# Kernel tuning notes

Measured on AMD Instinct MI355X. Metric: run time of the kernel, lower is better.

The kernel has to match this reference:

```python
import jax, jax.numpy as jnp
import numpy as np

ROW_PENALTY = 1.0
BIG = 9999.0
K = 8  # torch.topk(scores, 8, largest=False)


def _completion_loss(X, H, C, Mf, M):
    # X,H,C: [T,D] float; Mf: float mask; M: int mask (constant)
    T, D = H.shape
    diff = H[:, None, :] - H[None, :, :]                 # [T,T,D]
    # masked_select condition: (M[i]*M[j]) >= 0 per feature
    P = (Mf[:, None, :] * Mf[None, :, :]) >= 0           # [T,T,D] bool
    Pf = P.astype(H.dtype)
    n = Pf.sum(-1)                                       # [T,T] masked count
    s1 = (Pf * diff).sum(-1)                             # masked sum
    s2 = (Pf * diff * diff).sum(-1)                      # masked sum of squares
    mean = s1 / n
    # torch.var default is unbiased (n-1 denominator)
    var = (s2 - n * mean * mean) / (n - 1.0)
    # score only computed when i != j and (M[i] != M[j]).any(); else stays 9999
    valid = (M[:, None, :] != M[None, :, :]).any(-1) & (~jnp.eye(T, dtype=bool))
    scores = jnp.where(valid, jnp.sqrt(jnp.where(valid, var, 1.0)), BIG)
    # smallest-K via top_k on negated scores
    neg_vals, idx = jax.lax.top_k(-scores, K)            # [T,K]
    topk = -neg_vals
    w = jax.nn.softmax(-topk, axis=-1)                   # Softmax(dim=0) over the K-vector
    d2 = H[:, None, :] - H[idx]                          # [T,K,D]
    norms = jnp.sqrt((d2 * d2).sum(-1))                  # torch.norm(H[i]-H[j])
    row_loss = (w * norms).sum()
    mse = jnp.sum((X * Mf - (H - C) * Mf) ** 2)          # MSELoss(reduction='sum')
    return mse + ROW_PENALTY * row_loss


def setup_inputs() -> dict:
    key = jax.random.key(0)
    k1, k2, k3, k4 = jax.random.split(key, 4)
    T, D = 512, 256
    X = jax.random.normal(k1, (T, D), jnp.float32)
    H = jax.random.normal(k2, (T, D), jnp.float32)
    C = jax.random.normal(k3, (T, D), jnp.float32)
    M = jax.random.randint(k4, (T, D), 0, 2, jnp.int32)  # binary observation mask
    return {"X": X, "H": H, "C": C, "M": M, "T": T}


def reference(X, H, C, M, T):
    Mf = M.astype(X.dtype)
    return _completion_loss(X, H, C, Mf, M)
```

## Files before the change

kernel.cpp:

```cpp
#include <hip/hip_runtime.h>
#include <math.h>

#define TT 512
#define DD 256
#define BIGF 9999.0f
#define KK 8

typedef unsigned long long ull;
typedef __attribute__((ext_vector_type(8))) short s16x8;
typedef __attribute__((ext_vector_type(4))) float f32x4;

#define HB_OFF   0
#define G_OFF    262144
#define A_OFF    1310720
#define B_OFF    1312768
#define MB_OFF   1314816
#define MSEP_OFF 1331200

__device__ __forceinline__ unsigned short toBf16(float f) {
  unsigned int u = __float_as_uint(f);
  unsigned int r = u + 0x7FFFu + ((u >> 16) & 1u);
  return (unsigned short)(r >> 16);
}

__global__ __launch_bounds__(256) void prep_kernel(
    const float* __restrict__ X, const float* __restrict__ H,
    const float* __restrict__ C, const int* __restrict__ M,
    unsigned short* __restrict__ Hb, float* __restrict__ A,
    float* __restrict__ B, ull* __restrict__ MB, float* __restrict__ MSEP4,
    float* __restrict__ out) {
  const int b = blockIdx.x;
  const int t = threadIdx.x;
  const int wid = t >> 6, lane = t & 63;
  const int i0 = 4 * b;
  if (b == 0 && t == 0) out[0] = 0.0f;

  __shared__ float sA[4][4], sB[4][4], sM[4][4];
#pragma unroll
  for (int r = 0; r < 4; ++r) {
    const int row = i0 + r;
    const int idx = row * DD + t;
    const float x = X[idx], h = H[idx], c = C[idx];
    const int m = M[idx];
    const int dstk = t ^ ((row & 7) << 3);
    Hb[row * DD + dstk] = toBf16(h);
    const float e = m ? (x - h + c) : 0.0f;
    float pm = e * e, ph = h, ph2 = h * h;
#pragma unroll
    for (int s = 1; s < 64; s <<= 1) {
      pm  += __shfl_xor(pm, s);
      ph  += __shfl_xor(ph, s);
      ph2 += __shfl_xor(ph2, s);
    }
    const ull bal = __ballot(m != 0);
    if (lane == 0) {
      sA[r][wid] = ph; sB[r][wid] = ph2; sM[r][wid] = pm;
      MB[row * 4 + wid] = bal;
    }
  }
  __syncthreads();
  if (t < 4) {
    A[i0 + t] = sA[t][0] + sA[t][1] + sA[t][2] + sA[t][3];
    B[i0 + t] = sB[t][0] + sB[t][1] + sB[t][2] + sB[t][3];
  }
  if (t == 0) {
    float ms = 0.0f;
#pragma unroll
    for (int r = 0; r < 4; ++r)
#pragma unroll
      for (int wq = 0; wq < 4; ++wq) ms += sM[r][wq];
    MSEP4[b] = ms;
  }
}

__global__ __launch_bounds__(256, 2) void gram_kernel(
    const unsigned short* __restrict__ Hb, float* __restrict__ G) {
  __shared__ unsigned short At[64 * 256];
  __shared__ unsigned short Bt[64 * 256];
  const int t = threadIdx.x;
  const int lane = t & 63;
  const int wv = t >> 6;
  const int bx = blockIdx.x & 7, by = blockIdx.x >> 3;
  const int i0 = 64 * by, j0 = 64 * bx;

  {
    const s16x8* __restrict__ sa = (const s16x8*)(Hb + i0 * DD);
    const s16x8* __restrict__ sb = (const s16x8*)(Hb + j0 * DD);
    s16x8 va[8], vb[8];
#pragma unroll
    for (int q = 0; q < 8; ++q) va[q] = sa[q * 256 + t];
#pragma unroll
    for (int q = 0; q < 8; ++q) vb[q] = sb[q * 256 + t];
    s16x8* da = (s16x8*)At;
    s16x8* db = (s16x8*)Bt;
#pragma unroll
    for (int q = 0; q < 8; ++q) da[q * 256 + t] = va[q];
#pragma unroll
    for (int q = 0; q < 8; ++q) db[q * 256 + t] = vb[q];
  }
  __syncthreads();

  const int wr = wv >> 1, wc = wv & 1;
  const int frow = lane & 15;
  const int kgrp = lane >> 4;
  const f32x4 zero = {0.f, 0.f, 0.f, 0.f};
  f32x4 acc[2][2];
  acc[0][0] = zero; acc[0][1] = zero; acc[1][0] = zero; acc[1][1] = zero;

#pragma unroll
  for (int ks = 0; ks < 8; ++ks) {
    s16x8 a[2], bfr[2];
#pragma unroll
    for (int m = 0; m < 2; ++m) {
      const int rr = 32 * wr + 16 * m + frow;
      const int g = (ks * 4 + kgrp) ^ (rr & 7);
      a[m] = *(const s16x8*)(At + rr * 256 + g * 8);
    }
#pragma unroll
    for (int n = 0; n < 2; ++n) {
      const int rr = 32 * wc + 16 * n + frow;
      const int g = (ks * 4 + kgrp) ^ (rr & 7);
      bfr[n] = *(const s16x8*)(Bt + rr * 256 + g * 8);
    }
#pragma unroll
    for (int m = 0; m < 2; ++m)
#pragma unroll
      for (int n = 0; n < 2; ++n)
        acc[m][n] = __builtin_amdgcn_mfma_f32_16x16x32_bf16(
            a[m], bfr[n], acc[m][n], 0, 0, 0);
  }

  const int crow0 = (lane >> 4) * 4;
  const int ccol = lane & 15;
#pragma unroll
  for (int m = 0; m < 2; ++m)
#pragma unroll
    for (int n = 0; n < 2; ++n)
#pragma unroll
      for (int r = 0; r < 4; ++r) {
        const int gr = i0 + 32 * wr + 16 * m + crow0 + r;
        const int gc = j0 + 32 * wc + 16 * n + ccol;
        G[gr * TT + gc] = acc[m][n][r];
      }
}

__global__ __launch_bounds__(256) void score_kernel(
    const float* __restrict__ G, const float* __restrict__ A,
    const float* __restrict__ B, const ull* __restrict__ MB,
    const float* __restrict__ MSEP4, float* __restrict__ out) {
  __shared__ float dl[4][TT];
  __shared__ float nrm[4][TT];
  __shared__ float s_rl[4];
  const int b = blockIdx.x;
  const int t = threadIdx.x;
  const int wid = t >> 6, lane = t & 63;
  const int i0 = 4 * b;

  float2 gv[4];
#pragma unroll
  for (int r = 0; r < 4; ++r)
    gv[r] = *(const float2*)(G + (i0 + r) * TT + 2 * t);

  float ai[4], bi[4];
  ull mi[4][4];
#pragma unroll
  for (int r = 0; r < 4; ++r) {
    ai[r] = A[i0 + r];
    bi[r] = B[i0 + r];
#pragma unroll
    for (int c = 0; c < 4; ++c) mi[r][c] = MB[(i0 + r) * 4 + c];
  }

#pragma unroll
  for (int jj = 0; jj < 2; ++jj) {
    const int j = 2 * t + jj;
    const float aj = A[j], bj = B[j];
    const ull m0 = MB[j * 4 + 0], m1 = MB[j * 4 + 1],
              m2 = MB[j * 4 + 2], m3 = MB[j * 4 + 3];
#pragma unroll
    for (int r = 0; r < 4; ++r) {
      const float dot = jj ? gv[r].y : gv[r].x;
      const float s2 = bi[r] + bj - 2.0f * dot;
      const float s1 = ai[r] - aj;
      const float var = (s2 - s1 * s1 * (1.0f / DD)) * (1.0f / (DD - 1));
      const bool diff = (m0 != mi[r][0]) | (m1 != mi[r][1]) |
                        (m2 != mi[r][2]) | (m3 != mi[r][3]);
      const bool valid = diff && (j != i0 + r);
      dl[r][j] = valid ? sqrtf(fmaxf(var, 0.0f)) : BIGF;
      nrm[r][j] = sqrtf(fmaxf(s2, 0.0f));
    }
  }
  __syncthreads();

  {
    const int w = wid;
    float cv[8];
#pragma unroll
    for (int c = 0; c < 8; ++c) cv[c] = dl[w][lane + 64 * c];

    float kv[KK];
    int ki[KK];
#pragma unroll
    for (int k = 0; k < KK; ++k) {
      float bv = cv[0];
      int bc = 0;
#pragma unroll
      for (int c = 1; c < 8; ++c) {
        if (cv[c] < bv) { bv = cv[c]; bc = c; }
      }
      int bidx = lane + 64 * bc;
#pragma unroll
      for (int s = 1; s < 64; s <<= 1) {
        const float ov = __shfl_xor(bv, s);
        const int oi = __shfl_xor(bidx, s);
        if (ov < bv || (ov == bv && oi < bidx)) { bv = ov; bidx = oi; }
      }
      kv[k] = bv;
      ki[k] = bidx;
      const int csel = bidx >> 6;
      const bool mine = (bidx & 63) == lane;
#pragma unroll
      for (int c = 0; c < 8; ++c) {
        if (mine && c == csel) cv[c] = BIGF;
      }
    }
    float wsum = 0.0f, rl = 0.0f;
#pragma unroll
    for (int k = 0; k < KK; ++k) {
      const float e = expf(kv[0] - kv[k]);
      wsum += e;
      rl += e * nrm[w][ki[k]];
    }
    if (lane == 0) s_rl[w] = rl / wsum;
  }
  __syncthreads();

  if (t == 0)
    atomicAdd(out, s_rl[0] + s_rl[1] + s_rl[2] + s_rl[3] + MSEP4[b]);
}

extern "C" void kernel_launch(void* const* d_in, const int* in_sizes, int n_in,
                              void* d_out, int out_size, void* d_ws, size_t ws_size,
                              hipStream_t stream) {
  const float* X = (const float*)d_in[0];
  const float* H = (const float*)d_in[1];
  const float* C = (const float*)d_in[2];
  const int* M = (const int*)d_in[3];
  float* out = (float*)d_out;

  char* ws = (char*)d_ws;
  unsigned short* Hb = (unsigned short*)(ws + HB_OFF);
  float* G = (float*)(ws + G_OFF);
  float* A = (float*)(ws + A_OFF);
  float* B = (float*)(ws + B_OFF);
  ull* MB = (ull*)(ws + MB_OFF);
  float* MSEP4 = (float*)(ws + MSEP_OFF);

  prep_kernel<<<128, 256, 0, stream>>>(X, H, C, M, Hb, A, B, MB, MSEP4, out);
  gram_kernel<<<64, 256, 0, stream>>>(Hb, G);
  score_kernel<<<128, 256, 0, stream>>>(G, A, B, MB, MSEP4, out);
}
```

Measured before the change: 23.15 us.

## Fuse prep into gram kernel, converting H to bf16 on the fly

```diff
diff --git a/kernel.cpp b/kernel.cpp
--- a/kernel.cpp
+++ b/kernel.cpp
@@ -10,12 +10,11 @@
 typedef __attribute__((ext_vector_type(8))) short s16x8;
 typedef __attribute__((ext_vector_type(4))) float f32x4;
 
-#define HB_OFF   0
-#define G_OFF    262144
-#define A_OFF    1310720
-#define B_OFF    1312768
-#define MB_OFF   1314816
-#define MSEP_OFF 1331200
+#define G_OFF    0
+#define A_OFF    1048576
+#define B_OFF    1050624
+#define MB_OFF   1052672
+#define MSEP_OFF 1069056
 
 __device__ __forceinline__ unsigned short toBf16(float f) {
   unsigned int u = __float_as_uint(f);
@@ -23,80 +22,90 @@
   return (unsigned short)(r >> 16);
 }
 
-__global__ __launch_bounds__(256) void prep_kernel(
+__global__ __launch_bounds__(256, 2) void gramprep_kernel(
     const float* __restrict__ X, const float* __restrict__ H,
     const float* __restrict__ C, const int* __restrict__ M,
-    unsigned short* __restrict__ Hb, float* __restrict__ A,
-    float* __restrict__ B, ull* __restrict__ MB, float* __restrict__ MSEP4,
+    float* __restrict__ G, float* __restrict__ A, float* __restrict__ B,
+    ull* __restrict__ MB, float* __restrict__ MSEP64,
     float* __restrict__ out) {
-  const int b = blockIdx.x;
-  const int t = threadIdx.x;
-  const int wid = t >> 6, lane = t & 63;
-  const int i0 = 4 * b;
-  if (b == 0 && t == 0) out[0] = 0.0f;
-
-  __shared__ float sA[4][4], sB[4][4], sM[4][4];
-#pragma unroll
-  for (int r = 0; r < 4; ++r) {
-    const int row = i0 + r;
-    const int idx = row * DD + t;
-    const float x = X[idx], h = H[idx], c = C[idx];
-    const int m = M[idx];
-    const int dstk = t ^ ((row & 7) << 3);
-    Hb[row * DD + dstk] = toBf16(h);
-    const float e = m ? (x - h + c) : 0.0f;
-    float pm = e * e, ph = h, ph2 = h * h;
-#pragma unroll
-    for (int s = 1; s < 64; s <<= 1) {
-      pm  += __shfl_xor(pm, s);
-      ph  += __shfl_xor(ph, s);
-      ph2 += __shfl_xor(ph2, s);
-    }
-    const ull bal = __ballot(m != 0);
-    if (lane == 0) {
-      sA[r][wid] = ph; sB[r][wid] = ph2; sM[r][wid] = pm;
-      MB[row * 4 + wid] = bal;
-    }
-  }
-  __syncthreads();
-  if (t < 4) {
-    A[i0 + t] = sA[t][0] + sA[t][1] + sA[t][2] + sA[t][3];
-    B[i0 + t] = sB[t][0] + sB[t][1] + sB[t][2] + sB[t][3];
-  }
-  if (t == 0) {
-    float ms = 0.0f;
-#pragma unroll
-    for (int r = 0; r < 4; ++r)
-#pragma unroll
-      for (int wq = 0; wq < 4; ++wq) ms += sM[r][wq];
-    MSEP4[b] = ms;
-  }
-}
-
-__global__ __launch_bounds__(256, 2) void gram_kernel(
-    const unsigned short* __restrict__ Hb, float* __restrict__ G) {
   __shared__ unsigned short At[64 * 256];
   __shared__ unsigned short Bt[64 * 256];
+  __shared__ float sm[4];
+
   const int t = threadIdx.x;
-  const int lane = t & 63;
-  const int wv = t >> 6;
+  const int lane = t & 63, wv = t >> 6;
   const int bx = blockIdx.x & 7, by = blockIdx.x >> 3;
   const int i0 = 64 * by, j0 = 64 * bx;
+  if (blockIdx.x == 0 && t == 0) out[0] = 0.0f;
 
   {
-    const s16x8* __restrict__ sa = (const s16x8*)(Hb + i0 * DD);
-    const s16x8* __restrict__ sb = (const s16x8*)(Hb + j0 * DD);
-    s16x8 va[8], vb[8];
-#pragma unroll
-    for (int q = 0; q < 8; ++q) va[q] = sa[q * 256 + t];
-#pragma unroll
-    for (int q = 0; q < 8; ++q) vb[q] = sb[q * 256 + t];
-    s16x8* da = (s16x8*)At;
-    s16x8* db = (s16x8*)Bt;
-#pragma unroll
-    for (int q = 0; q < 8; ++q) da[q * 256 + t] = va[q];
-#pragma unroll
-    for (int q = 0; q < 8; ++q) db[q * 256 + t] = vb[q];
+    const float4* __restrict__ H4 = (const float4*)H;
+    const int k0 = lane * 4;
+    const int koff = (k0 & 7);
+#pragma unroll
+    for (int it = 0; it < 16; ++it) {
+      const int r = it * 4 + wv;
+      {
+        const float4 v = H4[(i0 + r) * 64 + lane];
+        ushort4 w;
+        w.x = toBf16(v.x); w.y = toBf16(v.y);
+        w.z = toBf16(v.z); w.w = toBf16(v.w);
+        const int g = (k0 >> 3) ^ (r & 7);
+        *(ushort4*)(At + r * 256 + g * 8 + koff) = w;
+      }
+      {
+        const float4 v = H4[(j0 + r) * 64 + lane];
+        ushort4 w;
+        w.x = toBf16(v.x); w.y = toBf16(v.y);
+        w.z = toBf16(v.z); w.w = toBf16(v.w);
+        const int g = (k0 >> 3) ^ (r & 7);
+        *(ushort4*)(Bt + r * 256 + g * 8 + koff) = w;
+      }
+    }
+  }
+
+  if (bx == by) {
+    const float4* __restrict__ H4 = (const float4*)H;
+    const float4* __restrict__ X4 = (const float4*)X;
+    const float4* __restrict__ C4 = (const float4*)C;
+    const int4*  __restrict__ M4 = (const int4*)M;
+    float mseAcc = 0.0f;
+#pragma unroll 2
+    for (int rr = 0; rr < 16; ++rr) {
+      const int row = i0 + wv * 16 + rr;
+      const float4 h4 = H4[row * 64 + lane];
+      const float4 x4 = X4[row * 64 + lane];
+      const float4 c4 = C4[row * 64 + lane];
+      const int4  m4 = M4[row * 64 + lane];
+      float pa = (h4.x + h4.y) + (h4.z + h4.w);
+      float pb = h4.x * h4.x + h4.y * h4.y + h4.z * h4.z + h4.w * h4.w;
+      const float e0 = x4.x - h4.x + c4.x;
+      const float e1 = x4.y - h4.y + c4.y;
+      const float e2 = x4.z - h4.z + c4.z;
+      const float e3 = x4.w - h4.w + c4.w;
+      float pe = (m4.x ? e0 * e0 : 0.f) + (m4.y ? e1 * e1 : 0.f) +
+                 (m4.z ? e2 * e2 : 0.f) + (m4.w ? e3 * e3 : 0.f);
+#pragma unroll
+      for (int s = 1; s < 64; s <<= 1) {
+        pa += __shfl_xor(pa, s);
+        pb += __shfl_xor(pb, s);
+        pe += __shfl_xor(pe, s);
+      }
+      const ull b0 = __ballot(m4.x != 0);
+      const ull b1 = __ballot(m4.y != 0);
+      const ull b2 = __ballot(m4.z != 0);
+      const ull b3 = __ballot(m4.w != 0);
+      if (lane == 0) {
+        A[row] = pa;
+        B[row] = pb;
+        MB[row * 4 + 0] = b0; MB[row * 4 + 1] = b1;
+        MB[row * 4 + 2] = b2; MB[row * 4 + 3] = b3;
+        mseAcc += pe;
+      }
+    }
+    if (lane == 0) sm[wv] = mseAcc;
+    __syncthreads();
+    if (t == 0) MSEP64[by] = sm[0] + sm[1] + sm[2] + sm[3];
   }
   __syncthreads();
 
@@ -147,7 +156,7 @@
 __global__ __launch_bounds__(256) void score_kernel(
     const float* __restrict__ G, const float* __restrict__ A,
     const float* __restrict__ B, const ull* __restrict__ MB,
-    const float* __restrict__ MSEP4, float* __restrict__ out) {
+    const float* __restrict__ MSEP64, float* __restrict__ out) {
   __shared__ float dl[4][TT];
   __shared__ float nrm[4][TT];
   __shared__ float s_rl[4];
@@ -235,8 +244,11 @@
   }
   __syncthreads();
 
-  if (t == 0)
-    atomicAdd(out, s_rl[0] + s_rl[1] + s_rl[2] + s_rl[3] + MSEP4[b]);
+  if (t == 0) {
+    float part = s_rl[0] + s_rl[1] + s_rl[2] + s_rl[3];
+    if ((b & 15) == 0) part += MSEP64[b >> 4];
+    atomicAdd(out, part);
+  }
 }
 
 extern "C" void kernel_launch(void* const* d_in, const int* in_sizes, int n_in,
@@ -249,14 +261,12 @@
   float* out = (float*)d_out;
 
   char* ws = (char*)d_ws;
-  unsigned short* Hb = (unsigned short*)(ws + HB_OFF);
   float* G = (float*)(ws + G_OFF);
   float* A = (float*)(ws + A_OFF);
   float* B = (float*)(ws + B_OFF);
   ull* MB = (ull*)(ws + MB_OFF);
-  float* MSEP4 = (float*)(ws + MSEP_OFF);
-
-  prep_kernel<<<128, 256, 0, stream>>>(X, H, C, M, Hb, A, B, MB, MSEP4, out);
-  gram_kernel<<<64, 256, 0, stream>>>(Hb, G);
-  score_kernel<<<128, 256, 0, stream>>>(G, A, B, MB, MSEP4, out);
-}
+  float* MSEP64 = (float*)(ws + MSEP_OFF);
+
+  gramprep_kernel<<<64, 256, 0, stream>>>(X, H, C, M, G, A, B, MB, MSEP64, out);
+  score_kernel<<<128, 256, 0, stream>>>(G, A, B, MB, MSEP64, out);
+}
```

Measured after the change: 27.02 us. +16.7%, slower.

## Shrink gram and score tiles to fill more CUs; vectorize prep kernel

Applied to the files above, without the earlier changes.

```diff
diff --git a/kernel.cpp b/kernel.cpp
--- a/kernel.cpp
+++ b/kernel.cpp
@@ -29,142 +29,130 @@
     unsigned short* __restrict__ Hb, float* __restrict__ A,
     float* __restrict__ B, ull* __restrict__ MB, float* __restrict__ MSEP4,
     float* __restrict__ out) {
+  __shared__ float sm[4];
   const int b = blockIdx.x;
   const int t = threadIdx.x;
-  const int wid = t >> 6, lane = t & 63;
-  const int i0 = 4 * b;
+  const int wv = t >> 6, lane = t & 63;
+  const int row = 4 * b + wv;
   if (b == 0 && t == 0) out[0] = 0.0f;
 
-  __shared__ float sA[4][4], sB[4][4], sM[4][4];
-#pragma unroll
-  for (int r = 0; r < 4; ++r) {
-    const int row = i0 + r;
-    const int idx = row * DD + t;
-    const float x = X[idx], h = H[idx], c = C[idx];
-    const int m = M[idx];
-    const int dstk = t ^ ((row & 7) << 3);
-    Hb[row * DD + dstk] = toBf16(h);
-    const float e = m ? (x - h + c) : 0.0f;
-    float pm = e * e, ph = h, ph2 = h * h;
-#pragma unroll
-    for (int s = 1; s < 64; s <<= 1) {
-      pm  += __shfl_xor(pm, s);
-      ph  += __shfl_xor(ph, s);
-      ph2 += __shfl_xor(ph2, s);
-    }
-    const ull bal = __ballot(m != 0);
-    if (lane == 0) {
-      sA[r][wid] = ph; sB[r][wid] = ph2; sM[r][wid] = pm;
-      MB[row * 4 + wid] = bal;
-    }
-  }
-  __syncthreads();
-  if (t < 4) {
-    A[i0 + t] = sA[t][0] + sA[t][1] + sA[t][2] + sA[t][3];
-    B[i0 + t] = sB[t][0] + sB[t][1] + sB[t][2] + sB[t][3];
-  }
-  if (t == 0) {
-    float ms = 0.0f;
-#pragma unroll
-    for (int r = 0; r < 4; ++r)
-#pragma unroll
-      for (int wq = 0; wq < 4; ++wq) ms += sM[r][wq];
-    MSEP4[b] = ms;
-  }
+  const float4 h4 = *(const float4*)(H + row * DD + 4 * lane);
+  const float4 x4 = *(const float4*)(X + row * DD + 4 * lane);
+  const float4 c4 = *(const float4*)(C + row * DD + 4 * lane);
+  const int4  m4 = *(const int4*)(M + row * DD + 4 * lane);
+
+  {
+    ushort4 w;
+    w.x = toBf16(h4.x); w.y = toBf16(h4.y);
+    w.z = toBf16(h4.z); w.w = toBf16(h4.w);
+    const int k0 = 4 * lane;
+    const int g = (k0 >> 3) ^ (row & 7);
+    *(ushort4*)(Hb + row * DD + g * 8 + (k0 & 7)) = w;
+  }
+
+  float pa = (h4.x + h4.y) + (h4.z + h4.w);
+  float pb = h4.x * h4.x + h4.y * h4.y + h4.z * h4.z + h4.w * h4.w;
+  const float e0 = x4.x - h4.x + c4.x;
+  const float e1 = x4.y - h4.y + c4.y;
+  const float e2 = x4.z - h4.z + c4.z;
+  const float e3 = x4.w - h4.w + c4.w;
+  float pe = (m4.x ? e0 * e0 : 0.f) + (m4.y ? e1 * e1 : 0.f) +
+             (m4.z ? e2 * e2 : 0.f) + (m4.w ? e3 * e3 : 0.f);
+#pragma unroll
+  for (int s = 1; s < 64; s <<= 1) {
+    pa += __shfl_xor(pa, s);
+    pb += __shfl_xor(pb, s);
+    pe += __shfl_xor(pe, s);
+  }
+  const ull b0 = __ballot(m4.x != 0);
+  const ull b1 = __ballot(m4.y != 0);
+  const ull b2 = __ballot(m4.z != 0);
+  const ull b3 = __ballot(m4.w != 0);
+  if (lane == 0) {
+    A[row] = pa;
+    B[row] = pb;
+    MB[row * 4 + 0] = b0; MB[row * 4 + 1] = b1;
+    MB[row * 4 + 2] = b2; MB[row * 4 + 3] = b3;
+    sm[wv] = pe;
+  }
+  __syncthreads();
+  if (t == 0) MSEP4[b] = sm[0] + sm[1] + sm[2] + sm[3];
 }
 
 __global__ __launch_bounds__(256, 2) void gram_kernel(
     const unsigned short* __restrict__ Hb, float* __restrict__ G) {
-  __shared__ unsigned short At[64 * 256];
-  __shared__ unsigned short Bt[64 * 256];
+  __shared__ unsigned short At[32 * 256];
+  __shared__ unsigned short Bt[32 * 256];
   const int t = threadIdx.x;
   const int lane = t & 63;
   const int wv = t >> 6;
-  const int bx = blockIdx.x & 7, by = blockIdx.x >> 3;
-  const int i0 = 64 * by, j0 = 64 * bx;
+  const int bx = blockIdx.x & 15, by = blockIdx.x >> 4;
+  const int i0 = 32 * by, j0 = 32 * bx;
 
   {
     const s16x8* __restrict__ sa = (const s16x8*)(Hb + i0 * DD);
     const s16x8* __restrict__ sb = (const s16x8*)(Hb + j0 * DD);
-    s16x8 va[8], vb[8];
-#pragma unroll
-    for (int q = 0; q < 8; ++q) va[q] = sa[q * 256 + t];
-#pragma unroll
-    for (int q = 0; q < 8; ++q) vb[q] = sb[q * 256 + t];
+    s16x8 va[4], vb[4];
+#pragma unroll
+    for (int q = 0; q < 4; ++q) va[q] = sa[q * 256 + t];
+#pragma unroll
+    for (int q = 0; q < 4; ++q) vb[q] = sb[q * 256 + t];
     s16x8* da = (s16x8*)At;
     s16x8* db = (s16x8*)Bt;
 #pragma unroll
-    for (int q = 0; q < 8; ++q) da[q * 256 + t] = va[q];
-#pragma unroll
-    for (int q = 0; q < 8; ++q) db[q * 256 + t] = vb[q];
+    for (int q = 0; q < 4; ++q) da[q * 256 + t] = va[q];
+#pragma unroll
+    for (int q = 0; q < 4; ++q) db[q * 256 + t] = vb[q];
   }
   __syncthreads();
 
   const int wr = wv >> 1, wc = wv & 1;
   const int frow = lane & 15;
   const int kgrp = lane >> 4;
-  const f32x4 zero = {0.f, 0.f, 0.f, 0.f};
-  f32x4 acc[2][2];
-  acc[0][0] = zero; acc[0][1] = zero; acc[1][0] = zero; acc[1][1] = zero;
+  f32x4 acc = {0.f, 0.f, 0.f, 0.f};
 
 #pragma unroll
   for (int ks = 0; ks < 8; ++ks) {
-    s16x8 a[2], bfr[2];
-#pragma unroll
-    for (int m = 0; m < 2; ++m) {
-      const int rr = 32 * wr + 16 * m + frow;
-      const int g = (ks * 4 + kgrp) ^ (rr & 7);
-      a[m] = *(const s16x8*)(At + rr * 256 + g * 8);
-    }
-#pragma unroll
-    for (int n = 0; n < 2; ++n) {
-      const int rr = 32 * wc + 16 * n + frow;
-      const int g = (ks * 4 + kgrp) ^ (rr & 7);
-      bfr[n] = *(const s16x8*)(Bt + rr * 256 + g * 8);
-    }
-#pragma unroll
-    for (int m = 0; m < 2; ++m)
-#pragma unroll
-      for (int n = 0; n < 2; ++n)
-        acc[m][n] = __builtin_amdgcn_mfma_f32_16x16x32_bf16(
-            a[m], bfr[n], acc[m][n], 0, 0, 0);
+    const int ra = 16 * wr + frow;
+    const int ga = (ks * 4 + kgrp) ^ (ra & 7);
+    const s16x8 a = *(const s16x8*)(At + ra * 256 + ga * 8);
+    const int rb = 16 * wc + frow;
+    const int gb = (ks * 4 + kgrp) ^ (rb & 7);
+    const s16x8 bfr = *(const s16x8*)(Bt + rb * 256 + gb * 8);
+    acc = __builtin_amdgcn_mfma_f32_16x16x32_bf16(a, bfr, acc, 0, 0, 0);
   }
 
   const int crow0 = (lane >> 4) * 4;
   const int ccol = lane & 15;
 #pragma unroll
-  for (int m = 0; m < 2; ++m)
-#pragma unroll
-    for (int n = 0; n < 2; ++n)
-#pragma unroll
-      for (int r = 0; r < 4; ++r) {
-        const int gr = i0 + 32 * wr + 16 * m + crow0 + r;
-        const int gc = j0 + 32 * wc + 16 * n + ccol;
-        G[gr * TT + gc] = acc[m][n][r];
-      }
+  for (int r = 0; r < 4; ++r) {
+    const int gr = i0 + 16 * wr + crow0 + r;
+    const int gc = j0 + 16 * wc + ccol;
+    G[gr * TT + gc] = acc[r];
+  }
 }
 
 __global__ __launch_bounds__(256) void score_kernel(
     const float* __restrict__ G, const float* __restrict__ A,
     const float* __restrict__ B, const ull* __restrict__ MB,
     const float* __restrict__ MSEP4, float* __restrict__ out) {
-  __shared__ float dl[4][TT];
-  __shared__ float nrm[4][TT];
-  __shared__ float s_rl[4];
+  __shared__ float dl[2][TT];
+  __shared__ float nrm[2][TT];
+  __shared__ float s_rl[2];
   const int b = blockIdx.x;
   const int t = threadIdx.x;
   const int wid = t >> 6, lane = t & 63;
-  const int i0 = 4 * b;
-
-  float2 gv[4];
-#pragma unroll
-  for (int r = 0; r < 4; ++r)
+  const int i0 = 2 * b;
+
+  float2 gv[2];
+#pragma unroll
+  for (int r = 0; r < 2; ++r)
     gv[r] = *(const float2*)(G + (i0 + r) * TT + 2 * t);
 
-  float ai[4], bi[4];
-  ull mi[4][4];
-#pragma unroll
-  for (int r = 0; r < 4; ++r) {
+  float ai[2], bi[2];
+  ull mi[2][4];
+#pragma unroll
+  for (int r = 0; r < 2; ++r) {
     ai[r] = A[i0 + r];
     bi[r] = B[i0 + r];
 #pragma unroll
@@ -178,7 +166,7 @@
     const ull m0 = MB[j * 4 + 0], m1 = MB[j * 4 + 1],
               m2 = MB[j * 4 + 2], m3 = MB[j * 4 + 3];
 #pragma unroll
-    for (int r = 0; r < 4; ++r) {
+    for (int r = 0; r < 2; ++r) {
       const float dot = jj ? gv[r].y : gv[r].x;
       const float s2 = bi[r] + bj - 2.0f * dot;
       const float s1 = ai[r] - aj;
@@ -192,7 +180,7 @@
   }
   __syncthreads();
 
-  {
+  if (wid < 2) {
     const int w = wid;
     float cv[8];
 #pragma unroll
@@ -235,8 +223,11 @@
   }
   __syncthreads();
 
-  if (t == 0)
-    atomicAdd(out, s_rl[0] + s_rl[1] + s_rl[2] + s_rl[3] + MSEP4[b]);
+  if (t == 0) {
+    float part = s_rl[0] + s_rl[1];
+    if ((b & 1) == 0) part += MSEP4[b >> 1];
+    atomicAdd(out, part);
+  }
 }
 
 extern "C" void kernel_launch(void* const* d_in, const int* in_sizes, int n_in,
@@ -257,6 +248,6 @@
   float* MSEP4 = (float*)(ws + MSEP_OFF);
 
   prep_kernel<<<128, 256, 0, stream>>>(X, H, C, M, Hb, A, B, MB, MSEP4, out);
-  gram_kernel<<<64, 256, 0, stream>>>(Hb, G);
-  score_kernel<<<128, 256, 0, stream>>>(G, A, B, MB, MSEP4, out);
-}
+  gram_kernel<<<256, 256, 0, stream>>>(Hb, G);
+  score_kernel<<<256, 256, 0, stream>>>(G, A, B, MB, MSEP4, out);
+}
```

New measurement: 23.58 us. About the same (+1.9%).
